# Optimization experiments

Hardware: AMD Instinct MI355X
Metric: run time of the kernel (lower is better)

The kernel has to match this reference:

```python
import jax, jax.numpy as jnp
import numpy as np

K = 7            # context_window
PAD = K // 2
CENTER = (K * K) // 2  # 24 causal kernel positions kept per channel


def _window_cols(x):
    """x: (B, C, H, W) -> (B, C, K*K, H, W), kernel positions in row-major order
    (matches torch F.unfold channel-major / kernel-minor layout after reshape)."""
    B, C, H, W = x.shape
    xp = jnp.pad(x, ((0, 0), (0, 0), (PAD, PAD), (PAD, PAD)))
    return jnp.stack([xp[:, :, i:i + H, j:j + W]
                      for i in range(K) for j in range(K)], axis=2)


def setup_inputs() -> dict:
    key = jax.random.key(0)
    ks = jax.random.split(key, 4)
    B, C, H, W = 1, 30, 256, 256          # C = channels * n_thresholds = 3*10
    in_dim = C * K * K                     # 1470 MLP input features
    hidden = 2048
    out_dim = 3 * 2                        # channels * 2
    x = jax.random.normal(ks[0], (B, C, H, W), jnp.float32)
    x_ups = jax.random.normal(ks[1], (B, C, H, W), jnp.float32)
    W1 = jax.random.normal(ks[2], (in_dim, hidden), jnp.float32) * np.float32(1.0 / np.sqrt(in_dim))
    b1 = jnp.zeros((hidden,), jnp.float32)
    W2 = jax.random.normal(ks[3], (hidden, out_dim), jnp.float32) * np.float32(1.0 / np.sqrt(hidden))
    b2 = jnp.zeros((out_dim,), jnp.float32)
    return {"x": x, "x_ups": x_ups, "W1": W1, "b1": b1, "W2": W2, "b2": b2}


def reference(x, x_ups, W1, b1, W2, b2):
    B, C, H, W = x.shape
    N = B * H * W
    channels = 3
    # causal_unroll: keep only the first CENTER kernel positions of each channel
    cols = _window_cols(x)                                # (B, C, 49, H, W)
    causal = cols[:, :, :CENTER]                          # (B, C, 24, H, W)
    causal = causal.reshape(B, C * CENTER, H * W).transpose(0, 2, 1).reshape(N, C * CENTER)
    # ups_unroll: full window, then flat slice [:, C*CENTER:] as in torch code
    cols_u = _window_cols(x_ups)                          # (B, C, 49, H, W)
    ups = cols_u.reshape(B, C * K * K, H * W).transpose(0, 2, 1).reshape(N, C * K * K)
    ups = ups[:, C * CENTER:]                             # (N, 750)
    feat = jnp.concatenate([causal, ups], axis=1)         # (N, 1470)
    # MLP (stand-in for model_config.create): Linear -> ReLU -> Linear
    h = jax.nn.relu(feat @ W1 + b1)
    out = h @ W2 + b2                                     # (N, 6)
    out = out.reshape(B, H * W, channels, 2)
    mu = out[..., 0] * 255.0
    s = out[..., 1]
    scale = jnp.clip(s / (1.0 - s + 0.1) * 100.0, 1e-8, 1000.0)
    return jnp.stack([mu, scale], axis=3)                 # (B, H*W, 3, 2)
```

## Files before the change

kernel.cpp:

```cpp
#include <hip/hip_runtime.h>

typedef unsigned short ushort_t;
typedef unsigned int uint_t;
typedef _Float16 f16;
typedef __attribute__((ext_vector_type(8))) _Float16 f16x8;
typedef __attribute__((ext_vector_type(8))) unsigned short u16x8;
typedef __attribute__((ext_vector_type(4))) float f32x4;

#define IMG_S 264
#define IMG_H 262
#define PLANE (IMG_H * IMG_S)
#define NPLANES 61
#define KTOT 1472
#define KREAL 1470
#define NHID 2048
#define NPIX 65536
#define BM 256
#define BN 128
#define BK 32
#define KSTEPS (KTOT / BK)
#define SA 8.0f
#define SB 512.0f
#define INV_S (1.0f / (SA * SB))

__device__ __forceinline__ uint_t f16pair(float f) {
    f16 h = (f16)f;
    f16 l = (f16)(f - (float)h);
    union { f16 a; ushort_t b; } uh, ul;
    uh.a = h; ul.a = l;
    return (uint_t)uh.b | ((uint_t)ul.b << 16);
}

__global__ void pad_imgs(const float* __restrict__ x, const float* __restrict__ xu,
                         uint_t* __restrict__ img2) {
    int idx = blockIdx.x * 256 + threadIdx.x;
    if (idx >= NPLANES * PLANE) return;
    int plane = idx / PLANE;
    int e = idx - plane * PLANE;
    int i = e / IMG_S;
    int j = e - i * IMG_S;
    uint_t v = 0;
    if (plane < 60 && i >= 3 && i < 259 && j >= 3 && j < 259) {
        const float* src = (plane < 30) ? x : xu;
        int c = (plane < 30) ? plane : plane - 30;
        float f = SA * src[(size_t)c * 65536 + (size_t)(i - 3) * 256 + (j - 3)];
        v = f16pair(f);
    }
    img2[idx] = v;
}

__global__ void boff_kernel(int* __restrict__ boff) {
    int f = blockIdx.x * 256 + threadIdx.x;
    if (f >= KTOT) return;
    int off;
    if (f < 720) {
        int c = f / 24, p = f - c * 24;
        off = c * PLANE + (p / 7) * IMG_S + (p % 7);
    } else if (f < KREAL) {
        int c = f / 49, p = f - c * 49;
        off = (30 + c) * PLANE + (p / 7) * IMG_S + (p % 7);
    } else {
        off = 60 * PLANE;
    }
    boff[f] = off;
}

__global__ void w1t_kernel(const float* __restrict__ w1,
                           ushort_t* __restrict__ w1t_hi, ushort_t* __restrict__ w1t_lo) {
    __shared__ float tile[32][33];
    const int bk  = blockIdx.x % 46;
    const int bnh = blockIdx.x / 46;
    const int t = threadIdx.x;
    const int r = t >> 5, c = t & 31;
#pragma unroll
    for (int s = 0; s < 4; ++s) {
        int kk = bk * 32 + s * 8 + r;
        int nh = bnh * 32 + c;
        tile[s * 8 + r][c] = (kk < KREAL) ? SB * w1[(size_t)kk * NHID + nh] : 0.0f;
    }
    __syncthreads();
#pragma unroll
    for (int s = 0; s < 4; ++s) {
        int nh = bnh * 32 + s * 8 + r;
        int kk = bk * 32 + c;
        float v = tile[c][s * 8 + r];
        uint_t p = f16pair(v);
        w1t_hi[(size_t)nh * KTOT + kk] = (ushort_t)(p & 0xffffu);
        w1t_lo[(size_t)nh * KTOT + kk] = (ushort_t)(p >> 16);
    }
}

__global__ __launch_bounds__(256, 2)
void fused_gemm(const uint_t* __restrict__ img2,
                const ushort_t* __restrict__ w1t_hi,
                const ushort_t* __restrict__ w1t_lo,
                const int* __restrict__ boff,
                const float* __restrict__ b1,
                const float* __restrict__ w2,
                float* __restrict__ accum) {
    __shared__ ushort_t Ah[BM * BK];
    __shared__ ushort_t Al[BM * BK];
    __shared__ ushort_t Bh[BN * BK];
    __shared__ ushort_t Bl[BN * BK];

    const int tid  = threadIdx.x;
    const int bid  = blockIdx.x;
    const int brow = bid >> 4;
    const int bcol = bid & 15;
    const int lane = tid & 63;
    const int wid  = tid >> 6;
    const int wm = wid >> 1;
    const int wn = wid & 1;

    const int hwoff = brow * IMG_S + tid;
    int aaddr[4];
#pragma unroll
    for (int s = 0; s < 4; ++s)
        aaddr[s] = (tid * (BK * 2) + s * 16) ^ ((tid & 7) << 4);
    const int bn_ = tid >> 1;
    const int kh  = (tid & 1) * 16;
    int baddr[2];
#pragma unroll
    for (int s = 0; s < 2; ++s)
        baddr[s] = (bn_ * (BK * 2) + kh * 2 + s * 16) ^ ((bn_ & 7) << 4);
    const size_t bglob = (size_t)(bcol * BN + bn_) * KTOT + kh;

    f32x4 zero = {0.f, 0.f, 0.f, 0.f};
    f32x4 acc[8][4];
#pragma unroll
    for (int mi = 0; mi < 8; ++mi)
#pragma unroll
        for (int ni = 0; ni < 4; ++ni) acc[mi][ni] = zero;

    for (int kt = 0; kt < KSTEPS; ++kt) {
        __syncthreads();
        const size_t bsrc = bglob + kt * BK;
#pragma unroll
        for (int s = 0; s < 2; ++s) {
            u16x8 vh = *reinterpret_cast<const u16x8*>(w1t_hi + bsrc + s * 8);
            u16x8 vl = *reinterpret_cast<const u16x8*>(w1t_lo + bsrc + s * 8);
            *reinterpret_cast<u16x8*>((char*)Bh + baddr[s]) = vh;
            *reinterpret_cast<u16x8*>((char*)Bl + baddr[s]) = vl;
        }
        const int f0 = kt * BK;
#pragma unroll
        for (int s = 0; s < 4; ++s) {
            uint_t w[8];
#pragma unroll
            for (int i = 0; i < 8; ++i)
                w[i] = img2[boff[f0 + s * 8 + i] + hwoff];
            u16x8 hi, lo;
#pragma unroll
            for (int i = 0; i < 8; ++i) {
                hi[i] = (ushort_t)(w[i] & 0xffffu);
                lo[i] = (ushort_t)(w[i] >> 16);
            }
            *reinterpret_cast<u16x8*>((char*)Ah + aaddr[s]) = hi;
            *reinterpret_cast<u16x8*>((char*)Al + aaddr[s]) = lo;
        }
        __syncthreads();
        f16x8 bfh[4], bfl[4];
#pragma unroll
        for (int ni = 0; ni < 4; ++ni) {
            int n = wn * 64 + ni * 16 + (lane & 15);
            int bb = (n * (BK * 2) + (lane >> 4) * 16) ^ ((n & 7) << 4);
            bfh[ni] = *reinterpret_cast<const f16x8*>((char*)Bh + bb);
            bfl[ni] = *reinterpret_cast<const f16x8*>((char*)Bl + bb);
        }
#pragma unroll
        for (int mi = 0; mi < 8; ++mi) {
            int m = wm * 128 + mi * 16 + (lane & 15);
            int ab = (m * (BK * 2) + (lane >> 4) * 16) ^ ((m & 7) << 4);
            f16x8 afh = *reinterpret_cast<const f16x8*>((char*)Ah + ab);
            f16x8 afl = *reinterpret_cast<const f16x8*>((char*)Al + ab);
#pragma unroll
            for (int ni = 0; ni < 4; ++ni) {
                acc[mi][ni] = __builtin_amdgcn_mfma_f32_16x16x32_f16(
                    afh, bfh[ni], acc[mi][ni], 0, 0, 0);
                acc[mi][ni] = __builtin_amdgcn_mfma_f32_16x16x32_f16(
                    afh, bfl[ni], acc[mi][ni], 0, 0, 0);
                acc[mi][ni] = __builtin_amdgcn_mfma_f32_16x16x32_f16(
                    afl, bfh[ni], acc[mi][ni], 0, 0, 0);
            }
        }
    }

    const int pix0 = brow * BM;
    float b1v[4], w2v[4][6];
#pragma unroll
    for (int ni = 0; ni < 4; ++ni) {
        int n = bcol * BN + wn * 64 + ni * 16 + (lane & 15);
        b1v[ni] = b1[n];
#pragma unroll
        for (int o = 0; o < 6; ++o) w2v[ni][o] = w2[n * 6 + o];
    }
#pragma unroll
    for (int mi = 0; mi < 8; ++mi) {
        float p[4][6];
#pragma unroll
        for (int r = 0; r < 4; ++r)
#pragma unroll
            for (int o = 0; o < 6; ++o) p[r][o] = 0.f;
#pragma unroll
        for (int ni = 0; ni < 4; ++ni) {
#pragma unroll
            for (int r = 0; r < 4; ++r) {
                float hv = fmaxf(acc[mi][ni][r] * INV_S + b1v[ni], 0.0f);
#pragma unroll
                for (int o = 0; o < 6; ++o) p[r][o] += hv * w2v[ni][o];
            }
        }
#pragma unroll
        for (int r = 0; r < 4; ++r) {
#pragma unroll
            for (int o = 0; o < 6; ++o) {
                float v = p[r][o];
                v += __shfl_xor(v, 1, 16);
                v += __shfl_xor(v, 2, 16);
                v += __shfl_xor(v, 4, 16);
                v += __shfl_xor(v, 8, 16);
                int q = r * 6 + o;
                if ((lane & 15) == (q & 15)) {
                    int orow = wm * 128 + mi * 16 + (lane >> 4) * 4 + r;
                    atomicAdd(&accum[(size_t)(pix0 + orow) * 6 + o], v);
                }
            }
        }
    }
}

__global__ void transform_k(const float* __restrict__ accum, const float* __restrict__ b2,
                            float* __restrict__ out) {
    int n = blockIdx.x * 256 + threadIdx.x;
    if (n >= NPIX) return;
#pragma unroll
    for (int ch = 0; ch < 3; ++ch) {
        float m = accum[(size_t)n * 6 + ch * 2 + 0] + b2[ch * 2 + 0];
        float s = accum[(size_t)n * 6 + ch * 2 + 1] + b2[ch * 2 + 1];
        out[(size_t)n * 6 + ch * 2 + 0] = m * 255.0f;
        float denom = 1.0f - s + 0.1f;
        float sc = s / denom * 100.0f;
        sc = fminf(fmaxf(sc, 1e-8f), 1000.0f);
        out[(size_t)n * 6 + ch * 2 + 1] = sc;
    }
}

extern "C" void kernel_launch(void* const* d_in, const int* in_sizes, int n_in,
                              void* d_out, int out_size, void* d_ws, size_t ws_size,
                              hipStream_t stream) {
    const float* x  = (const float*)d_in[0];
    const float* xu = (const float*)d_in[1];
    const float* W1 = (const float*)d_in[2];
    const float* b1 = (const float*)d_in[3];
    const float* W2 = (const float*)d_in[4];
    const float* b2 = (const float*)d_in[5];
    float* out = (float*)d_out;
    char* ws = (char*)d_ws;

    const size_t OFF_W1H  = 16877056;
    const size_t OFF_W1L  = OFF_W1H + (size_t)NHID * KTOT * 2;
    const size_t OFF_ACC  = OFF_W1L + (size_t)NHID * KTOT * 2;
    const size_t OFF_BOFF = OFF_ACC + (size_t)NPIX * 6 * sizeof(float);
    uint_t* img2    = (uint_t*)ws;
    ushort_t* w1t_h = (ushort_t*)(ws + OFF_W1H);
    ushort_t* w1t_l = (ushort_t*)(ws + OFF_W1L);
    float* accum    = (float*)(ws + OFF_ACC);
    int* boff       = (int*)(ws + OFF_BOFF);
    (void)ws_size; (void)in_sizes; (void)n_in; (void)out_size;

    hipMemsetAsync(accum, 0, (size_t)NPIX * 6 * sizeof(float), stream);

    int padN = NPLANES * PLANE;
    pad_imgs<<<(padN + 255) / 256, 256, 0, stream>>>(x, xu, img2);
    boff_kernel<<<(KTOT + 255) / 256, 256, 0, stream>>>(boff);
    w1t_kernel<<<46 * 64, 256, 0, stream>>>(W1, w1t_h, w1t_l);
    fused_gemm<<<256 * 16, 256, 0, stream>>>(img2, w1t_h, w1t_l, boff, b1, W2, accum);
    transform_k<<<NPIX / 256, 256, 0, stream>>>(accum, b2, out);
}
```

Before: 1.502 ms.

## Prefetch next K-tile global loads into registers during MFMA compute

```diff
diff --git a/kernel.cpp b/kernel.cpp
--- a/kernel.cpp
+++ b/kernel.cpp
@@ -125,6 +125,19 @@
         baddr[s] = (bn_ * (BK * 2) + kh * 2 + s * 16) ^ ((bn_ & 7) << 4);
     const size_t bglob = (size_t)(bcol * BN + bn_) * KTOT + kh;
 
+    uint_t aw[4][8];
+    u16x8 bwh[2], bwl[2];
+#pragma unroll
+    for (int s = 0; s < 4; ++s)
+#pragma unroll
+        for (int i = 0; i < 8; ++i)
+            aw[s][i] = img2[boff[s * 8 + i] + hwoff];
+#pragma unroll
+    for (int s = 0; s < 2; ++s) {
+        bwh[s] = *reinterpret_cast<const u16x8*>(w1t_hi + bglob + s * 8);
+        bwl[s] = *reinterpret_cast<const u16x8*>(w1t_lo + bglob + s * 8);
+    }
+
     f32x4 zero = {0.f, 0.f, 0.f, 0.f};
     f32x4 acc[8][4];
 #pragma unroll
@@ -134,31 +147,39 @@
 
     for (int kt = 0; kt < KSTEPS; ++kt) {
         __syncthreads();
-        const size_t bsrc = bglob + kt * BK;
 #pragma unroll
         for (int s = 0; s < 2; ++s) {
-            u16x8 vh = *reinterpret_cast<const u16x8*>(w1t_hi + bsrc + s * 8);
-            u16x8 vl = *reinterpret_cast<const u16x8*>(w1t_lo + bsrc + s * 8);
-            *reinterpret_cast<u16x8*>((char*)Bh + baddr[s]) = vh;
-            *reinterpret_cast<u16x8*>((char*)Bl + baddr[s]) = vl;
-        }
-        const int f0 = kt * BK;
+            *reinterpret_cast<u16x8*>((char*)Bh + baddr[s]) = bwh[s];
+            *reinterpret_cast<u16x8*>((char*)Bl + baddr[s]) = bwl[s];
+        }
 #pragma unroll
         for (int s = 0; s < 4; ++s) {
-            uint_t w[8];
-#pragma unroll
-            for (int i = 0; i < 8; ++i)
-                w[i] = img2[boff[f0 + s * 8 + i] + hwoff];
             u16x8 hi, lo;
-#pragma unroll
-            for (int i = 0; i < 8; ++i) {
-                hi[i] = (ushort_t)(w[i] & 0xffffu);
-                lo[i] = (ushort_t)(w[i] >> 16);
+            uint_t* hp = reinterpret_cast<uint_t*>(&hi);
+            uint_t* lp = reinterpret_cast<uint_t*>(&lo);
+#pragma unroll
+            for (int i = 0; i < 4; ++i) {
+                hp[i] = __builtin_amdgcn_perm(aw[s][2 * i + 1], aw[s][2 * i], 0x05040100u);
+                lp[i] = __builtin_amdgcn_perm(aw[s][2 * i + 1], aw[s][2 * i], 0x07060302u);
             }
             *reinterpret_cast<u16x8*>((char*)Ah + aaddr[s]) = hi;
             *reinterpret_cast<u16x8*>((char*)Al + aaddr[s]) = lo;
         }
         __syncthreads();
+        if (kt + 1 < KSTEPS) {
+            const int f0n = (kt + 1) * BK;
+#pragma unroll
+            for (int s = 0; s < 4; ++s)
+#pragma unroll
+                for (int i = 0; i < 8; ++i)
+                    aw[s][i] = img2[boff[f0n + s * 8 + i] + hwoff];
+            const size_t bsrc = bglob + (size_t)(kt + 1) * BK;
+#pragma unroll
+            for (int s = 0; s < 2; ++s) {
+                bwh[s] = *reinterpret_cast<const u16x8*>(w1t_hi + bsrc + s * 8);
+                bwl[s] = *reinterpret_cast<const u16x8*>(w1t_lo + bsrc + s * 8);
+            }
+        }
         f16x8 bfh[4], bfl[4];
 #pragma unroll
         for (int ni = 0; ni < 4; ++ni) {
```

New measurement: 1.427 ms. 5.0% less time.
